# Kernel tuning notes

Hardware: AMD Instinct MI355X
Metric: run time of the kernel (lower is better)

Reference implementation:

```python
import jax, jax.numpy as jnp
import numpy as np

CH = 256  # channels

def setup_inputs() -> dict:
    key = jax.random.key(0)
    ks = jax.random.split(key, 9)
    B, H, W = 8, 64, 64
    c8, c2 = CH // 8, CH // 2
    s = lambda fan_in: 1.0 / np.sqrt(fan_in)
    return {
        "x": jax.random.normal(ks[0], (B, H, W, CH), dtype=jnp.float32),
        "Wq": jax.random.normal(ks[1], (CH, c8), dtype=jnp.float32) * s(CH),
        "bq": jnp.zeros((c8,), dtype=jnp.float32),
        "Wk": jax.random.normal(ks[2], (CH, c8), dtype=jnp.float32) * s(CH),
        "bk": jnp.zeros((c8,), dtype=jnp.float32),
        "Wv": jax.random.normal(ks[3], (CH, c2), dtype=jnp.float32) * s(CH),
        "bv": jnp.zeros((c2,), dtype=jnp.float32),
        "Wo": jax.random.normal(ks[4], (c2, CH), dtype=jnp.float32) * s(c2),
        "bo": jnp.zeros((CH,), dtype=jnp.float32),
    }

def reference(x, Wq, bq, Wk, bk, Wv, bv, Wo, bo):
    B, H, W, C = x.shape
    # 1x1 convs are per-pixel matmuls over the channel dim
    q = x @ Wq + bq                      # [B,H,W,C/8]
    k = x @ Wk + bk                      # [B,H,W,C/8]
    v = x @ Wv + bv                      # [B,H,W,C/2]
    N = H * W
    qf = q.reshape(B, N, -1)
    kf = k.reshape(B, N, -1)
    vf = v.reshape(B, N, -1)
    # full self-attention over flattened spatial positions (no scaling, per source)
    scores = jnp.einsum('bnd,bmd->bnm', qf, kf)   # [B,N,N]
    attn = jax.nn.softmax(scores, axis=-1)
    out = jnp.einsum('bnm,bmd->bnd', attn, vf)    # [B,N,C/2]
    out = out.reshape(B, H, W, -1)
    return out @ Wo + bo + x
```

## Files before the change

kernel.cpp:

```cpp
#include <hip/hip_runtime.h>

typedef __attribute__((ext_vector_type(8))) short short8;
typedef __attribute__((ext_vector_type(2))) float f32x2;
typedef __attribute__((ext_vector_type(4))) float f32x4;
typedef __attribute__((ext_vector_type(16))) float f32x16;

__device__ __forceinline__ unsigned short f2bf(float f) {
  unsigned int u = __float_as_uint(f);
  u += 0x7fffu + ((u >> 16) & 1u);
  return (unsigned short)(u >> 16);
}
__device__ __forceinline__ float bf2f(unsigned short h) {
  return __uint_as_float(((unsigned int)h) << 16);
}
__device__ __forceinline__ unsigned int cvtpk(float a, float b) {
  unsigned int r;
  asm("v_cvt_pk_bf16_f32 %0, %1, %2" : "=v"(r) : "v"(a), "v"(b));
  return r;
}
__device__ __forceinline__ float lo16f(unsigned int u) { return __uint_as_float(u << 16); }
__device__ __forceinline__ float hi16f(unsigned int u) { return __uint_as_float(u & 0xffff0000u); }
__device__ __forceinline__ short8 ld8(const unsigned short* p) {
  return *(const short8*)p;
}
__device__ __forceinline__ int swap23(int x) {
  return (x & 0x13) | ((x & 4) << 1) | ((x & 8) >> 1);
}
#define MFMA(a, b, c) __builtin_amdgcn_mfma_f32_16x16x32_bf16((a), (b), (c), 0, 0, 0)
#define MFMA32(a, b, c) __builtin_amdgcn_mfma_f32_32x32x16_bf16((a), (b), (c), 0, 0, 0)
#define LOG2E 1.4426950408889634f

typedef const __attribute__((address_space(1))) unsigned int* gas_u32p;
typedef __attribute__((address_space(3))) unsigned int* las_u32p;

__global__ void prep_weights(const float* __restrict__ Wq, const float* __restrict__ Wk,
                             const float* __restrict__ Wv, const float* __restrict__ Wo,
                             unsigned short* __restrict__ Wth, unsigned short* __restrict__ Wtl,
                             unsigned short* __restrict__ WoT) {
  int idx = blockIdx.x * 256 + threadIdx.x;
  if (idx < 192 * 256) {
    int o = idx >> 8, c = idx & 255;
    float w = (o < 32) ? Wq[c * 32 + o] : (o < 64) ? Wk[c * 32 + (o - 32)] : Wv[c * 128 + (o - 64)];
    unsigned short h = f2bf(w);
    Wth[idx] = h;
    Wtl[idx] = f2bf(w - bf2f(h));
  } else if (idx < 192 * 256 + 256 * 128) {
    int j = idx - 192 * 256;
    int c = j >> 7, d = j & 127;
    WoT[j] = f2bf(Wo[d * 256 + c]);
  }
}

__global__ __launch_bounds__(256) void proj_qkv(
    const float* __restrict__ x,
    const unsigned short* __restrict__ Wth, const unsigned short* __restrict__ Wtl,
    const float* __restrict__ bq, const float* __restrict__ bk, const float* __restrict__ bv,
    unsigned short* __restrict__ qh, unsigned short* __restrict__ qlo,
    unsigned short* __restrict__ KVF) {
  __shared__ unsigned short xsh[32][264];
  __shared__ unsigned short xsl[32][264];
  const int pix0 = blockIdx.x * 32;
  const int b = pix0 >> 12;
  const int nloc0 = pix0 & 4095;
  const int tid = threadIdx.x;

#pragma unroll
  for (int i = 0; i < 8; ++i) {
    int chunk = i * 256 + tid;
    int row = chunk >> 6;
    int c4 = (chunk & 63) * 4;
    float4 v = *(const float4*)(x + (size_t)(pix0 + row) * 256 + c4);
    unsigned int h01 = cvtpk(v.x, v.y), h23 = cvtpk(v.z, v.w);
    unsigned int l01 = cvtpk(v.x - lo16f(h01), v.y - hi16f(h01));
    unsigned int l23 = cvtpk(v.z - lo16f(h23), v.w - hi16f(h23));
    uint2 hp, lp;
    hp.x = h01; hp.y = h23;
    lp.x = l01; lp.y = l23;
    *(uint2*)&xsh[row][c4] = hp;
    *(uint2*)&xsl[row][c4] = lp;
  }
  __syncthreads();

  const int wave = tid >> 6, lane = tid & 63, l = lane & 15, qd = lane >> 4;
#pragma unroll
  for (int si = 0; si < 3; ++si) {
    const int sub = wave + si * 4;
    const int outc0 = sub * 16;
    if (si == 0) {
      const int outc = outc0 + l;
      const float bias = (outc < 32) ? bq[outc] : bk[outc - 32];
      f32x4 acc[2];
      acc[0] = (f32x4){bias, bias, bias, bias};
      acc[1] = (f32x4){bias, bias, bias, bias};
#pragma unroll
      for (int kc = 0; kc < 8; ++kc) {
        short8 whf = ld8(Wth + (size_t)(outc0 + l) * 256 + kc * 32 + qd * 8);
        short8 wlf = ld8(Wtl + (size_t)(outc0 + l) * 256 + kc * 32 + qd * 8);
#pragma unroll
        for (int m = 0; m < 2; ++m) {
          short8 xhf = ld8(&xsh[m * 16 + l][kc * 32 + qd * 8]);
          short8 xlf = ld8(&xsl[m * 16 + l][kc * 32 + qd * 8]);
          acc[m] = MFMA(xlf, whf, acc[m]);
          acc[m] = MFMA(xhf, wlf, acc[m]);
          acc[m] = MFMA(xhf, whf, acc[m]);
        }
      }
      if (outc < 32) {
#pragma unroll
        for (int m = 0; m < 2; ++m)
#pragma unroll
          for (int r = 0; r < 4; ++r) {
            const size_t pixel = (size_t)pix0 + m * 16 + 4 * qd + r;
            float val = acc[m][r] * LOG2E;
            unsigned int hp = cvtpk(val, val);
            float res = val - lo16f(hp);
            qh[pixel * 32 + outc] = (unsigned short)hp;
            qlo[pixel * 32 + outc] = (unsigned short)cvtpk(res, res);
          }
      } else {
        const int kd = outc - 32;
        const int step = kd >> 4, hh = (kd >> 3) & 1, e = kd & 7;
#pragma unroll
        for (int m = 0; m < 2; ++m)
#pragma unroll
          for (int r = 0; r < 4; ++r) {
            const int nl = nloc0 + m * 16 + 4 * qd + r;
            const int nt = nl >> 6, j = nl & 63, kt = j >> 5;
            const int lpos = swap23(j & 31);
            const size_t koff = (size_t)(b * 64 + nt) * 12288 +
                                (kt * 2 + step) * 512 + (hh * 32 + lpos) * 8 + e;
            float val = acc[m][r];
            unsigned int hp = cvtpk(val, val);
            float res = val - lo16f(hp);
            KVF[koff] = (unsigned short)hp;
            KVF[koff + 2048] = (unsigned short)cvtpk(res, res);
          }
      }
    } else {
      const int dv0 = outc0 - 64;
      const float b0 = bv[dv0 + 4 * qd + 0], b1 = bv[dv0 + 4 * qd + 1];
      const float b2 = bv[dv0 + 4 * qd + 2], b3 = bv[dv0 + 4 * qd + 3];
      f32x4 acc[2];
      acc[0] = (f32x4){b0, b1, b2, b3};
      acc[1] = (f32x4){b0, b1, b2, b3};
#pragma unroll
      for (int kc = 0; kc < 8; ++kc) {
        short8 whf = ld8(Wth + (size_t)(outc0 + l) * 256 + kc * 32 + qd * 8);
#pragma unroll
        for (int m = 0; m < 2; ++m) {
          short8 xhf = ld8(&xsh[m * 16 + l][kc * 32 + qd * 8]);
          acc[m] = MFMA(whf, xhf, acc[m]);
        }
      }
#pragma unroll
      for (int m = 0; m < 2; ++m)
#pragma unroll
        for (int r = 0; r < 4; ++r) {
          const int dv = dv0 + 4 * qd + r;
          const int dt = dv >> 5, lam = dv & 31;
          const int nl = nloc0 + m * 16 + l;
          const int nt = nl >> 6, j = nl & 63;
          const int ks = j >> 4, hh = (j >> 3) & 1, e = j & 7;
          const size_t voff = (size_t)(b * 64 + nt) * 12288 + 4096 +
                              (dt * 4 + ks) * 512 + (hh * 32 + lam) * 8 + e;
          KVF[voff] = (unsigned short)cvtpk(acc[m][r], acc[m][r]);
        }
    }
  }
}

__device__ __forceinline__ void stage_kv(const unsigned short* __restrict__ src,
                                         unsigned short* dst, int wave, int lane) {
#pragma unroll
  for (int i = 0; i < 6; ++i) {
    const int c = wave * 6 + i;
    __builtin_amdgcn_global_load_lds(
        (gas_u32p)(const void*)(src + c * 512 + lane * 8),
        (las_u32p)(void*)(dst + c * 512), 16, 0, 0);
  }
}

__global__ __launch_bounds__(256, 2) void flash_attn(
    const unsigned short* __restrict__ qh, const unsigned short* __restrict__ qlo,
    const unsigned short* __restrict__ KVF, unsigned short* __restrict__ opart,
    float* __restrict__ lstat) {
  __shared__ unsigned short kv[2][12288];
  const int b = blockIdx.x & 7;
  const int r7 = blockIdx.x >> 3;
  const int tile = r7 & 15;
  const int split = r7 >> 4;
  const int wave = threadIdx.x >> 6;
  const int lane = threadIdx.x & 63;
  const int lam = lane & 31;
  const int h = lane >> 5;
  const int m0 = tile * 256 + wave * 64;
  const int nt0 = split * 16;

  const unsigned short* qh_b = qh + (size_t)b * 4096 * 32;
  const unsigned short* ql_b = qlo + (size_t)b * 4096 * 32;
  const unsigned short* kv_b = KVF + (size_t)b * 64 * 12288;

  short8 qhf[2][2], qlf[2][2];
#pragma unroll
  for (int t = 0; t < 2; ++t)
#pragma unroll
    for (int step = 0; step < 2; ++step) {
      size_t off = (size_t)(m0 + t * 32 + lam) * 32 + step * 16 + h * 8;
      qhf[t][step] = ld8(qh_b + off);
      qlf[t][step] = ld8(ql_b + off);
    }

  f32x16 acc0[4], acc1[4];
#pragma unroll
  for (int dt = 0; dt < 4; ++dt)
#pragma unroll
    for (int e = 0; e < 16; ++e) { acc0[dt][e] = 0.f; acc1[dt][e] = 0.f; }
  f32x2 lr0 = (f32x2){0.f, 0.f}, lr1 = (f32x2){0.f, 0.f};

  stage_kv(kv_b + (size_t)nt0 * 12288, &kv[0][0], wave, lane);
  __syncthreads();

  int cur = 0;
#pragma unroll 1
  for (int it = 0; it < 16; ++it) {
    if (it < 15)
      stage_kv(kv_b + (size_t)(nt0 + it + 1) * 12288, &kv[cur ^ 1][0], wave, lane);

    const unsigned short* cb = &kv[cur][0];
#pragma unroll
    for (int kt = 0; kt < 2; ++kt) {
      short8 khf[2], klf[2];
#pragma unroll
      for (int step = 0; step < 2; ++step) {
        khf[step] = *(const short8*)(cb + (kt * 2 + step) * 512 + lane * 8);
        klf[step] = *(const short8*)(cb + 2048 + (kt * 2 + step) * 512 + lane * 8);
      }
      f32x16 z0, z1;
#pragma unroll
      for (int e = 0; e < 16; ++e) { z0[e] = 0.f; z1[e] = 0.f; }
      __builtin_amdgcn_s_setprio(1);
#pragma unroll
      for (int step = 0; step < 2; ++step) {
        z0 = MFMA32(klf[step], qhf[0][step], z0);
        z0 = MFMA32(khf[step], qlf[0][step], z0);
        z0 = MFMA32(khf[step], qhf[0][step], z0);
      }
#pragma unroll
      for (int step = 0; step < 2; ++step) {
        z1 = MFMA32(klf[step], qhf[1][step], z1);
        z1 = MFMA32(khf[step], qlf[1][step], z1);
        z1 = MFMA32(khf[step], qhf[1][step], z1);
      }
      __builtin_amdgcn_s_setprio(0);
      unsigned int pp0[8], pp1[8];
#pragma unroll
      for (int g = 0; g < 8; ++g) {
        float a0 = __builtin_amdgcn_exp2f(z0[2 * g]);
        float a1 = __builtin_amdgcn_exp2f(z0[2 * g + 1]);
        lr0 += (f32x2){a0, a1};
        pp0[g] = cvtpk(a0, a1);
        float c0 = __builtin_amdgcn_exp2f(z1[2 * g]);
        float c1 = __builtin_amdgcn_exp2f(z1[2 * g + 1]);
        lr1 += (f32x2){c0, c1};
        pp1[g] = cvtpk(c0, c1);
      }
      __builtin_amdgcn_s_setprio(1);
#pragma unroll
      for (int kss = 0; kss < 2; ++kss) {
        union { unsigned int u[4]; short8 v; } pf0, pf1;
#pragma unroll
        for (int j = 0; j < 4; ++j) {
          pf0.u[j] = pp0[4 * kss + j];
          pf1.u[j] = pp1[4 * kss + j];
        }
        const int ks = kt * 2 + kss;
#pragma unroll
        for (int dt = 0; dt < 4; ++dt) {
          short8 vfrag = *(const short8*)(cb + 4096 + (dt * 4 + ks) * 512 + lane * 8);
          acc0[dt] = MFMA32(vfrag, pf0.v, acc0[dt]);
          acc1[dt] = MFMA32(vfrag, pf1.v, acc1[dt]);
        }
      }
      __builtin_amdgcn_s_setprio(0);
    }
    __syncthreads();
    cur ^= 1;
  }

  {
    const float lrun = lr0.x + lr0.y;
    const float ltot = lrun + __shfl_xor(lrun, 32);
    const int grow = b * 4096 + m0 + lam;
    if (h == 0) lstat[split * 32768 + grow] = ltot;
    const size_t obase = ((size_t)split * 32768 + grow) * 128;
#pragma unroll
    for (int dt = 0; dt < 4; ++dt)
#pragma unroll
      for (int g = 0; g < 8; ++g) {
        int r = 2 * g;
        int dv = dt * 32 + (r & 3) + 8 * (r >> 2) + 4 * h;
        *(unsigned int*)(opart + obase + dv) = cvtpk(acc0[dt][r], acc0[dt][r + 1]);
      }
  }
  {
    const float lrun = lr1.x + lr1.y;
    const float ltot = lrun + __shfl_xor(lrun, 32);
    const int grow = b * 4096 + m0 + 32 + lam;
    if (h == 0) lstat[split * 32768 + grow] = ltot;
    const size_t obase = ((size_t)split * 32768 + grow) * 128;
#pragma unroll
    for (int dt = 0; dt < 4; ++dt)
#pragma unroll
      for (int g = 0; g < 8; ++g) {
        int r = 2 * g;
        int dv = dt * 32 + (r & 3) + 8 * (r >> 2) + 4 * h;
        *(unsigned int*)(opart + obase + dv) = cvtpk(acc1[dt][r], acc1[dt][r + 1]);
      }
  }
}

__global__ __launch_bounds__(256) void combine_splits(
    const unsigned short* __restrict__ opart, const float* __restrict__ lstat,
    unsigned short* __restrict__ ao) {
  const int tid = threadIdx.x;
  const int row = blockIdx.x * 16 + (tid >> 4);
  const int col = (tid & 15) * 8;
  float den = lstat[row] + lstat[32768 + row] + lstat[65536 + row] + lstat[98304 + row];
  float inv = 1.f / den;
  float o[8] = {0.f, 0.f, 0.f, 0.f, 0.f, 0.f, 0.f, 0.f};
#pragma unroll
  for (int s = 0; s < 4; ++s) {
    uint4 v = *(const uint4*)(opart + ((size_t)s * 32768 + row) * 128 + col);
    unsigned int uu[4] = {v.x, v.y, v.z, v.w};
#pragma unroll
    for (int j = 0; j < 4; ++j) {
      o[2 * j]     += bf2f((unsigned short)(uu[j] & 0xffff));
      o[2 * j + 1] += bf2f((unsigned short)(uu[j] >> 16));
    }
  }
  uint4 outv;
  outv.x = cvtpk(o[0] * inv, o[1] * inv);
  outv.y = cvtpk(o[2] * inv, o[3] * inv);
  outv.z = cvtpk(o[4] * inv, o[5] * inv);
  outv.w = cvtpk(o[6] * inv, o[7] * inv);
  *(uint4*)(ao + (size_t)row * 128 + col) = outv;
}

__global__ __launch_bounds__(256) void out_proj(
    const unsigned short* __restrict__ ao, const unsigned short* __restrict__ WoT,
    const float* __restrict__ bo, const float* __restrict__ x, float* __restrict__ out) {
  const int pix0 = blockIdx.x * 64;
  const int wave = threadIdx.x >> 6, lane = threadIdx.x & 63, l = lane & 15, qd = lane >> 4;
  const int base = pix0 + wave * 16;
  short8 af[4];
#pragma unroll
  for (int kc = 0; kc < 4; ++kc)
    af[kc] = ld8(ao + (size_t)(base + l) * 128 + kc * 32 + qd * 8);
#pragma unroll
  for (int sub = 0; sub < 16; ++sub) {
    const int c0 = sub * 16 + 4 * qd;
    float4 bb = *(const float4*)(bo + c0);
    f32x4 acc = (f32x4){bb.x, bb.y, bb.z, bb.w};
#pragma unroll
    for (int kc = 0; kc < 4; ++kc) {
      short8 wf = ld8(WoT + (size_t)(sub * 16 + l) * 128 + kc * 32 + qd * 8);
      acc = MFMA(wf, af[kc], acc);
    }
    float4 xv = *(const float4*)(x + (size_t)(base + l) * 256 + c0);
    float4 res;
    res.x = acc[0] + xv.x;
    res.y = acc[1] + xv.y;
    res.z = acc[2] + xv.z;
    res.w = acc[3] + xv.w;
    *(float4*)(out + (size_t)(base + l) * 256 + c0) = res;
  }
}

extern "C" void kernel_launch(void* const* d_in, const int* in_sizes, int n_in,
                              void* d_out, int out_size, void* d_ws, size_t ws_size,
                              hipStream_t stream) {
  const float* x  = (const float*)d_in[0];
  const float* Wq = (const float*)d_in[1];
  const float* bq = (const float*)d_in[2];
  const float* Wk = (const float*)d_in[3];
  const float* bk = (const float*)d_in[4];
  const float* Wv = (const float*)d_in[5];
  const float* bv = (const float*)d_in[6];
  const float* Wo = (const float*)d_in[7];
  const float* bo = (const float*)d_in[8];

  char* ws = (char*)d_ws;
  unsigned short* qh  = (unsigned short*)(ws + 0);
  unsigned short* qlo = (unsigned short*)(ws + 2097152);
  unsigned short* KVF = (unsigned short*)(ws + 4194304);
  unsigned short* ao  = (unsigned short*)(ws + 16777216);
  unsigned short* Wth = (unsigned short*)(ws + 25165824);
  unsigned short* Wtl = (unsigned short*)(ws + 25264128);
  unsigned short* WoT = (unsigned short*)(ws + 25362432);
  float*          lst = (float*)(ws + 25493504);
  unsigned short* opart = (unsigned short*)d_out;

  prep_weights<<<320, 256, 0, stream>>>(Wq, Wk, Wv, Wo, Wth, Wtl, WoT);
  proj_qkv<<<1024, 256, 0, stream>>>(x, Wth, Wtl, bq, bk, bv, qh, qlo, KVF);
  flash_attn<<<512, 256, 0, stream>>>(qh, qlo, KVF, opart, lst);
  combine_splits<<<2048, 256, 0, stream>>>(opart, lst, ao);
  out_proj<<<512, 256, 0, stream>>>(ao, WoT, bo, x, (float*)d_out);
}
```

Baseline: 200.4 us.

## Use single fp16 MFMA for QK scores instead of split-bf16 hi/lo products

Q and K are now stored as single fp16 values instead of bf16 high/low pairs. The score computation drops from three bf16 MFMAs per step to one fp16 MFMA. This removes the qlo buffer and the K low-part storage, which shrinks the per-tile KV buffer, the LDS staging and the global traffic. The inner loop is also reordered so the second half's score MFMAs are issued alongside the first half's PV MFMAs. The trade-off is lower score accuracy from fp16's 10-bit mantissa, and overflow risk, since the softmax applies exp2 without subtracting a max.

```diff
diff --git a/kernel.cpp b/kernel.cpp
--- a/kernel.cpp
+++ b/kernel.cpp
@@ -1,6 +1,7 @@
 #include <hip/hip_runtime.h>
 
 typedef __attribute__((ext_vector_type(8))) short short8;
+typedef __attribute__((ext_vector_type(8))) _Float16 half8;
 typedef __attribute__((ext_vector_type(2))) float f32x2;
 typedef __attribute__((ext_vector_type(4))) float f32x4;
 typedef __attribute__((ext_vector_type(16))) float f32x16;
@@ -18,16 +19,25 @@
   asm("v_cvt_pk_bf16_f32 %0, %1, %2" : "=v"(r) : "v"(a), "v"(b));
   return r;
 }
+__device__ __forceinline__ unsigned short f2h(float f) {
+  unsigned int r;
+  asm("v_cvt_f16_f32 %0, %1" : "=v"(r) : "v"(f));
+  return (unsigned short)r;
+}
 __device__ __forceinline__ float lo16f(unsigned int u) { return __uint_as_float(u << 16); }
 __device__ __forceinline__ float hi16f(unsigned int u) { return __uint_as_float(u & 0xffff0000u); }
 __device__ __forceinline__ short8 ld8(const unsigned short* p) {
   return *(const short8*)p;
 }
+__device__ __forceinline__ half8 ld8h(const unsigned short* p) {
+  return *(const half8*)p;
+}
 __device__ __forceinline__ int swap23(int x) {
   return (x & 0x13) | ((x & 4) << 1) | ((x & 8) >> 1);
 }
 #define MFMA(a, b, c) __builtin_amdgcn_mfma_f32_16x16x32_bf16((a), (b), (c), 0, 0, 0)
 #define MFMA32(a, b, c) __builtin_amdgcn_mfma_f32_32x32x16_bf16((a), (b), (c), 0, 0, 0)
+#define MFMA32H(a, b, c) __builtin_amdgcn_mfma_f32_32x32x16_f16((a), (b), (c), 0, 0, 0)
 #define LOG2E 1.4426950408889634f
 
 typedef const __attribute__((address_space(1))) unsigned int* gas_u32p;
@@ -55,8 +65,7 @@
     const float* __restrict__ x,
     const unsigned short* __restrict__ Wth, const unsigned short* __restrict__ Wtl,
     const float* __restrict__ bq, const float* __restrict__ bk, const float* __restrict__ bv,
-    unsigned short* __restrict__ qh, unsigned short* __restrict__ qlo,
-    unsigned short* __restrict__ KVF) {
+    unsigned short* __restrict__ qh, unsigned short* __restrict__ KVF) {
   __shared__ unsigned short xsh[32][264];
   __shared__ unsigned short xsl[32][264];
   const int pix0 = blockIdx.x * 32;
@@ -111,11 +120,7 @@
 #pragma unroll
           for (int r = 0; r < 4; ++r) {
             const size_t pixel = (size_t)pix0 + m * 16 + 4 * qd + r;
-            float val = acc[m][r] * LOG2E;
-            unsigned int hp = cvtpk(val, val);
-            float res = val - lo16f(hp);
-            qh[pixel * 32 + outc] = (unsigned short)hp;
-            qlo[pixel * 32 + outc] = (unsigned short)cvtpk(res, res);
+            qh[pixel * 32 + outc] = f2h(acc[m][r] * LOG2E);
           }
       } else {
         const int kd = outc - 32;
@@ -127,13 +132,9 @@
             const int nl = nloc0 + m * 16 + 4 * qd + r;
             const int nt = nl >> 6, j = nl & 63, kt = j >> 5;
             const int lpos = swap23(j & 31);
-            const size_t koff = (size_t)(b * 64 + nt) * 12288 +
+            const size_t koff = (size_t)(b * 64 + nt) * 10240 +
                                 (kt * 2 + step) * 512 + (hh * 32 + lpos) * 8 + e;
-            float val = acc[m][r];
-            unsigned int hp = cvtpk(val, val);
-            float res = val - lo16f(hp);
-            KVF[koff] = (unsigned short)hp;
-            KVF[koff + 2048] = (unsigned short)cvtpk(res, res);
+            KVF[koff] = f2h(acc[m][r]);
           }
       }
     } else {
@@ -161,7 +162,7 @@
           const int nl = nloc0 + m * 16 + l;
           const int nt = nl >> 6, j = nl & 63;
           const int ks = j >> 4, hh = (j >> 3) & 1, e = j & 7;
-          const size_t voff = (size_t)(b * 64 + nt) * 12288 + 4096 +
+          const size_t voff = (size_t)(b * 64 + nt) * 10240 + 2048 +
                               (dt * 4 + ks) * 512 + (hh * 32 + lam) * 8 + e;
           KVF[voff] = (unsigned short)cvtpk(acc[m][r], acc[m][r]);
         }
@@ -172,8 +173,8 @@
 __device__ __forceinline__ void stage_kv(const unsigned short* __restrict__ src,
                                          unsigned short* dst, int wave, int lane) {
 #pragma unroll
-  for (int i = 0; i < 6; ++i) {
-    const int c = wave * 6 + i;
+  for (int i = 0; i < 5; ++i) {
+    const int c = wave * 5 + i;
     __builtin_amdgcn_global_load_lds(
         (gas_u32p)(const void*)(src + c * 512 + lane * 8),
         (las_u32p)(void*)(dst + c * 512), 16, 0, 0);
@@ -181,10 +182,10 @@
 }
 
 __global__ __launch_bounds__(256, 2) void flash_attn(
-    const unsigned short* __restrict__ qh, const unsigned short* __restrict__ qlo,
+    const unsigned short* __restrict__ qh,
     const unsigned short* __restrict__ KVF, unsigned short* __restrict__ opart,
     float* __restrict__ lstat) {
-  __shared__ unsigned short kv[2][12288];
+  __shared__ unsigned short kv[2][10240];
   const int b = blockIdx.x & 7;
   const int r7 = blockIdx.x >> 3;
   const int tile = r7 & 15;
@@ -197,18 +198,14 @@
   const int nt0 = split * 16;
 
   const unsigned short* qh_b = qh + (size_t)b * 4096 * 32;
-  const unsigned short* ql_b = qlo + (size_t)b * 4096 * 32;
-  const unsigned short* kv_b = KVF + (size_t)b * 64 * 12288;
-
-  short8 qhf[2][2], qlf[2][2];
+  const unsigned short* kv_b = KVF + (size_t)b * 64 * 10240;
+
+  half8 qf[2][2];
 #pragma unroll
   for (int t = 0; t < 2; ++t)
 #pragma unroll
-    for (int step = 0; step < 2; ++step) {
-      size_t off = (size_t)(m0 + t * 32 + lam) * 32 + step * 16 + h * 8;
-      qhf[t][step] = ld8(qh_b + off);
-      qlf[t][step] = ld8(ql_b + off);
-    }
+    for (int step = 0; step < 2; ++step)
+      qf[t][step] = ld8h(qh_b + (size_t)(m0 + t * 32 + lam) * 32 + step * 16 + h * 8);
 
   f32x16 acc0[4], acc1[4];
 #pragma unroll
@@ -217,72 +214,91 @@
     for (int e = 0; e < 16; ++e) { acc0[dt][e] = 0.f; acc1[dt][e] = 0.f; }
   f32x2 lr0 = (f32x2){0.f, 0.f}, lr1 = (f32x2){0.f, 0.f};
 
-  stage_kv(kv_b + (size_t)nt0 * 12288, &kv[0][0], wave, lane);
+  stage_kv(kv_b + (size_t)nt0 * 10240, &kv[0][0], wave, lane);
   __syncthreads();
 
   int cur = 0;
 #pragma unroll 1
   for (int it = 0; it < 16; ++it) {
     if (it < 15)
-      stage_kv(kv_b + (size_t)(nt0 + it + 1) * 12288, &kv[cur ^ 1][0], wave, lane);
+      stage_kv(kv_b + (size_t)(nt0 + it + 1) * 10240, &kv[cur ^ 1][0], wave, lane);
 
     const unsigned short* cb = &kv[cur][0];
-#pragma unroll
-    for (int kt = 0; kt < 2; ++kt) {
-      short8 khf[2], klf[2];
-#pragma unroll
-      for (int step = 0; step < 2; ++step) {
-        khf[step] = *(const short8*)(cb + (kt * 2 + step) * 512 + lane * 8);
-        klf[step] = *(const short8*)(cb + 2048 + (kt * 2 + step) * 512 + lane * 8);
-      }
-      f32x16 z0, z1;
-#pragma unroll
-      for (int e = 0; e < 16; ++e) { z0[e] = 0.f; z1[e] = 0.f; }
-      __builtin_amdgcn_s_setprio(1);
-#pragma unroll
-      for (int step = 0; step < 2; ++step) {
-        z0 = MFMA32(klf[step], qhf[0][step], z0);
-        z0 = MFMA32(khf[step], qlf[0][step], z0);
-        z0 = MFMA32(khf[step], qhf[0][step], z0);
-      }
-#pragma unroll
-      for (int step = 0; step < 2; ++step) {
-        z1 = MFMA32(klf[step], qhf[1][step], z1);
-        z1 = MFMA32(khf[step], qlf[1][step], z1);
-        z1 = MFMA32(khf[step], qhf[1][step], z1);
-      }
-      __builtin_amdgcn_s_setprio(0);
-      unsigned int pp0[8], pp1[8];
-#pragma unroll
-      for (int g = 0; g < 8; ++g) {
-        float a0 = __builtin_amdgcn_exp2f(z0[2 * g]);
-        float a1 = __builtin_amdgcn_exp2f(z0[2 * g + 1]);
-        lr0 += (f32x2){a0, a1};
-        pp0[g] = cvtpk(a0, a1);
-        float c0 = __builtin_amdgcn_exp2f(z1[2 * g]);
-        float c1 = __builtin_amdgcn_exp2f(z1[2 * g + 1]);
-        lr1 += (f32x2){c0, c1};
-        pp1[g] = cvtpk(c0, c1);
-      }
-      __builtin_amdgcn_s_setprio(1);
-#pragma unroll
-      for (int kss = 0; kss < 2; ++kss) {
-        union { unsigned int u[4]; short8 v; } pf0, pf1;
-#pragma unroll
-        for (int j = 0; j < 4; ++j) {
-          pf0.u[j] = pp0[4 * kss + j];
-          pf1.u[j] = pp1[4 * kss + j];
-        }
-        const int ks = kt * 2 + kss;
-#pragma unroll
-        for (int dt = 0; dt < 4; ++dt) {
-          short8 vfrag = *(const short8*)(cb + 4096 + (dt * 4 + ks) * 512 + lane * 8);
-          acc0[dt] = MFMA32(vfrag, pf0.v, acc0[dt]);
-          acc1[dt] = MFMA32(vfrag, pf1.v, acc1[dt]);
-        }
-      }
-      __builtin_amdgcn_s_setprio(0);
-    }
+
+    half8 k0a = ld8h(cb + 0 * 512 + lane * 8);
+    half8 k0b = ld8h(cb + 1 * 512 + lane * 8);
+    f32x16 z0, z1;
+#pragma unroll
+    for (int e = 0; e < 16; ++e) { z0[e] = 0.f; z1[e] = 0.f; }
+    __builtin_amdgcn_s_setprio(1);
+    z0 = MFMA32H(k0a, qf[0][0], z0);
+    z0 = MFMA32H(k0b, qf[0][1], z0);
+    z1 = MFMA32H(k0a, qf[1][0], z1);
+    z1 = MFMA32H(k0b, qf[1][1], z1);
+    __builtin_amdgcn_s_setprio(0);
+    unsigned int ppA0[8], ppA1[8];
+#pragma unroll
+    for (int g = 0; g < 8; ++g) {
+      float a0 = __builtin_amdgcn_exp2f(z0[2 * g]);
+      float a1 = __builtin_amdgcn_exp2f(z0[2 * g + 1]);
+      lr0 += (f32x2){a0, a1};
+      ppA0[g] = cvtpk(a0, a1);
+      float c0 = __builtin_amdgcn_exp2f(z1[2 * g]);
+      float c1 = __builtin_amdgcn_exp2f(z1[2 * g + 1]);
+      lr1 += (f32x2){c0, c1};
+      ppA1[g] = cvtpk(c0, c1);
+    }
+
+    half8 k1a = ld8h(cb + 2 * 512 + lane * 8);
+    half8 k1b = ld8h(cb + 3 * 512 + lane * 8);
+    f32x16 w0, w1;
+#pragma unroll
+    for (int e = 0; e < 16; ++e) { w0[e] = 0.f; w1[e] = 0.f; }
+    __builtin_amdgcn_s_setprio(1);
+    w0 = MFMA32H(k1a, qf[0][0], w0);
+    w0 = MFMA32H(k1b, qf[0][1], w0);
+    w1 = MFMA32H(k1a, qf[1][0], w1);
+    w1 = MFMA32H(k1b, qf[1][1], w1);
+#pragma unroll
+    for (int kss = 0; kss < 2; ++kss) {
+      union { unsigned int u[4]; short8 v; } pf0, pf1;
+#pragma unroll
+      for (int j = 0; j < 4; ++j) { pf0.u[j] = ppA0[4 * kss + j]; pf1.u[j] = ppA1[4 * kss + j]; }
+#pragma unroll
+      for (int dt = 0; dt < 4; ++dt) {
+        short8 vfrag = *(const short8*)(cb + 2048 + (dt * 4 + kss) * 512 + lane * 8);
+        acc0[dt] = MFMA32(vfrag, pf0.v, acc0[dt]);
+        acc1[dt] = MFMA32(vfrag, pf1.v, acc1[dt]);
+      }
+    }
+    __builtin_amdgcn_s_setprio(0);
+    unsigned int ppB0[8], ppB1[8];
+#pragma unroll
+    for (int g = 0; g < 8; ++g) {
+      float a0 = __builtin_amdgcn_exp2f(w0[2 * g]);
+      float a1 = __builtin_amdgcn_exp2f(w0[2 * g + 1]);
+      lr0 += (f32x2){a0, a1};
+      ppB0[g] = cvtpk(a0, a1);
+      float c0 = __builtin_amdgcn_exp2f(w1[2 * g]);
+      float c1 = __builtin_amdgcn_exp2f(w1[2 * g + 1]);
+      lr1 += (f32x2){c0, c1};
+      ppB1[g] = cvtpk(c0, c1);
+    }
+    __builtin_amdgcn_s_setprio(1);
+#pragma unroll
+    for (int kss = 0; kss < 2; ++kss) {
+      union { unsigned int u[4]; short8 v; } pf0, pf1;
+#pragma unroll
+      for (int j = 0; j < 4; ++j) { pf0.u[j] = ppB0[4 * kss + j]; pf1.u[j] = ppB1[4 * kss + j]; }
+#pragma unroll
+      for (int dt = 0; dt < 4; ++dt) {
+        short8 vfrag = *(const short8*)(cb + 2048 + (dt * 4 + 2 + kss) * 512 + lane * 8);
+        acc0[dt] = MFMA32(vfrag, pf0.v, acc0[dt]);
+        acc1[dt] = MFMA32(vfrag, pf1.v, acc1[dt]);
+      }
+    }
+    __builtin_amdgcn_s_setprio(0);
+
     __syncthreads();
     cur ^= 1;
   }
@@ -391,18 +407,17 @@
 
   char* ws = (char*)d_ws;
   unsigned short* qh  = (unsigned short*)(ws + 0);
-  unsigned short* qlo = (unsigned short*)(ws + 2097152);
-  unsigned short* KVF = (unsigned short*)(ws + 4194304);
-  unsigned short* ao  = (unsigned short*)(ws + 16777216);
-  unsigned short* Wth = (unsigned short*)(ws + 25165824);
-  unsigned short* Wtl = (unsigned short*)(ws + 25264128);
-  unsigned short* WoT = (unsigned short*)(ws + 25362432);
-  float*          lst = (float*)(ws + 25493504);
+  unsigned short* KVF = (unsigned short*)(ws + 2097152);
+  unsigned short* ao  = (unsigned short*)(ws + 12582912);
+  unsigned short* Wth = (unsigned short*)(ws + 20971520);
+  unsigned short* Wtl = (unsigned short*)(ws + 21069824);
+  unsigned short* WoT = (unsigned short*)(ws + 21168128);
+  float*          lst = (float*)(ws + 21233664);
   unsigned short* opart = (unsigned short*)d_out;
 
   prep_weights<<<320, 256, 0, stream>>>(Wq, Wk, Wv, Wo, Wth, Wtl, WoT);
-  proj_qkv<<<1024, 256, 0, stream>>>(x, Wth, Wtl, bq, bk, bv, qh, qlo, KVF);
-  flash_attn<<<512, 256, 0, stream>>>(qh, qlo, KVF, opart, lst);
+  proj_qkv<<<1024, 256, 0, stream>>>(x, Wth, Wtl, bq, bk, bv, qh, KVF);
+  flash_attn<<<512, 256, 0, stream>>>(qh, KVF, opart, lst);
   combine_splits<<<2048, 256, 0, stream>>>(opart, lst, ao);
   out_proj<<<512, 256, 0, stream>>>(ao, WoT, bo, x, (float*)d_out);
 }
```

New measurement: 191.4 us. -4.5%, faster.
